# Performance work log

Measured on AMD Instinct MI355X. Metric: run time of the kernel, lower is better.

Reference implementation:

```python
import jax, jax.numpy as jnp
import numpy as np

B, IN_DIM, C, H, W = 4, 64, 128, 64, 64
HW = H * W
EPS = 1e-5


def _conv(x, w, b, pad):
    y = jax.lax.conv_general_dilated(
        x, w, (1, 1), [(pad, pad), (pad, pad)],
        dimension_numbers=('NCHW', 'OIHW', 'NCHW'))
    return y + b[None, :, None, None]


def _ln_chw(x, g, b):
    # torch LayerNorm([C,H,W]): normalize over (C,H,W) per sample, affine per-element
    m = jnp.mean(x, axis=(1, 2, 3), keepdims=True)
    v = jnp.mean((x - m) ** 2, axis=(1, 2, 3), keepdims=True)
    return (x - m) * jax.lax.rsqrt(v + EPS) * g[None] + b[None]


def _lrelu(x):
    return jnp.where(x >= 0, x, 0.01 * x)


def setup_inputs():
    ks = jax.random.split(jax.random.key(0), 16)

    def n(i, shape, s):
        return jax.random.normal(ks[i], shape, jnp.float32) * s

    inp = {
        'f_e': n(0, (B, IN_DIM, H, W), 1.0),
        'f_i': n(1, (B, IN_DIM, H, W), 1.0),
        'w1': n(2, (C, IN_DIM, 3, 3), 0.04), 'b1': jnp.zeros((C,), jnp.float32),
        'g1': jnp.ones((C, H, W), jnp.float32), 'be1': jnp.zeros((C, H, W), jnp.float32),
        'w2': n(3, (C, IN_DIM, 3, 3), 0.04), 'b2': jnp.zeros((C,), jnp.float32),
        'g2': jnp.ones((C, H, W), jnp.float32), 'be2': jnp.zeros((C, H, W), jnp.float32),
        'W3': n(4, (HW, HW), 0.015), 'b3': jnp.zeros((HW,), jnp.float32),
        'W4': n(5, (C, C), 0.08), 'b4': jnp.zeros((C,), jnp.float32),
        'W5': n(6, (C, C), 0.08), 'b5': jnp.zeros((C,), jnp.float32),
        'w6a': n(7, (C, C, 1, 1), 0.08), 'b6a': jnp.zeros((C,), jnp.float32),
        'g6a': jnp.ones((C, H, W), jnp.float32), 'be6a': jnp.zeros((C, H, W), jnp.float32),
        'w6b': n(8, (C, C, 3, 3), 0.03), 'b6b': jnp.zeros((C,), jnp.float32),
        'g6b': jnp.ones((C, H, W), jnp.float32), 'be6b': jnp.zeros((C, H, W), jnp.float32),
        'wf': n(9, (IN_DIM, C, 1, 1), 0.08), 'bf': jnp.zeros((IN_DIM,), jnp.float32),
    }
    return inp


def reference(f_e, f_i, w1, b1, g1, be1, w2, b2, g2, be2, W3, b3, W4, b4,
              W5, b5, w6a, b6a, g6a, be6a, w6b, b6b, g6b, be6b, wf, bf):
    b_, _, h, w = f_e.shape
    c = w1.shape[0]
    hw = h * w

    # f_1: conv3x3 -> LN([C,H,W]) -> LeakyReLU -> b (hw) c
    x1 = _lrelu(_ln_chw(_conv(f_e, w1, b1, 1), g1, be1))
    f_e_1 = x1.transpose(0, 2, 3, 1).reshape(b_, hw, c)

    # f_2: conv3x3 -> LN -> LeakyReLU (stays b c h w)
    f_i_2 = _lrelu(_ln_chw(_conv(f_i, w2, b2, 1), g2, be2))

    # f_3: b c (hw) -> Linear(HW,HW) -> LeakyReLU
    f_i_3 = _lrelu(jnp.einsum('bcn,mn->bcm', f_i_2.reshape(b_, c, hw), W3) + b3)

    # f_4: b (hw) c -> Linear(C,C) -> LeakyReLU
    tok = f_i_2.transpose(0, 2, 3, 1).reshape(b_, hw, c)
    f_e_4 = _lrelu(jnp.einsum('bnc,dc->bnd', tok, W4) + b4)

    # unscaled single-head attention over hw tokens
    scores = jnp.einsum('bnc,bcm->bnm', f_e_4, f_i_3)   # (b, hw, hw)
    attn = jax.nn.softmax(scores, axis=-1)
    f_e_5_in = jnp.einsum('bnm,bmc->bnc', attn, f_e_1)

    # f_5: Linear(C,C) -> LeakyReLU -> b c h w
    f_e_5 = _lrelu(jnp.einsum('bnc,dc->bnd', f_e_5_in, W5) + b5)
    f_e_5 = f_e_5.reshape(b_, h, w, c).transpose(0, 3, 1, 2)

    # f_6: conv1x1 -> LN -> LReLU -> conv3x3 -> LN -> LReLU
    y = _lrelu(_ln_chw(_conv(f_i_2, w6a, b6a, 0), g6a, be6a))
    f_i_6 = _lrelu(_ln_chw(_conv(y, w6b, b6b, 1), g6b, be6b))

    f_e_7 = f_e_5 * f_i_6
    f_e_8 = _conv(f_e_7, wf, bf, 0)
    return (f_e_8, f_i_2)
```

## Files before the change

kernel.cpp:

```cpp
#include <hip/hip_runtime.h>

typedef unsigned short ushort_t;
typedef unsigned int uint_t;
typedef unsigned long long u64_t;

#define Bn 4
#define IND 64
#define Cn 128
#define Nn 4096
#define CN 524288
#define BUF 2097152

typedef __attribute__((ext_vector_type(8))) __bf16 bf16x8;
typedef __attribute__((ext_vector_type(4))) float f32x4;

__device__ __forceinline__ float b2f(ushort_t s) {
    return __uint_as_float(((uint_t)s) << 16);
}
__device__ __forceinline__ ushort_t f2b(float f) {
    uint_t u = __float_as_uint(f);
    uint_t r = u + 0x7fffu + ((u >> 16) & 1u);
    return (ushort_t)(r >> 16);
}
__device__ __forceinline__ void unpack8(uint4 u, float* f) {
    f[0] = __uint_as_float(u.x << 16); f[1] = __uint_as_float(u.x & 0xffff0000u);
    f[2] = __uint_as_float(u.y << 16); f[3] = __uint_as_float(u.y & 0xffff0000u);
    f[4] = __uint_as_float(u.z << 16); f[5] = __uint_as_float(u.z & 0xffff0000u);
    f[6] = __uint_as_float(u.w << 16); f[7] = __uint_as_float(u.w & 0xffff0000u);
}
__device__ __forceinline__ float lrelu(float x) { return x >= 0.f ? x : 0.01f * x; }

__device__ __forceinline__ float getv(const float* p, size_t i) { return p[i]; }
__device__ __forceinline__ float getv(const ushort_t* p, size_t i) { return b2f(p[i]); }
__device__ __forceinline__ float4 get4(const float* p, size_t i) { return *(const float4*)(p + i); }
__device__ __forceinline__ float4 get4(const ushort_t* p, size_t i) {
    ushort4 u = *(const ushort4*)(p + i);
    float4 f = {b2f(u.x), b2f(u.y), b2f(u.z), b2f(u.w)};
    return f;
}
__device__ __forceinline__ void stv(float* p, float v) { *p = v; }
__device__ __forceinline__ void stv(ushort_t* p, float v) { *p = f2b(v); }

__device__ __forceinline__ uint4 pack8(float4 a, float4 b) {
    uint4 r;
    r.x = (uint_t)f2b(a.x) | ((uint_t)f2b(a.y) << 16);
    r.y = (uint_t)f2b(a.z) | ((uint_t)f2b(a.w) << 16);
    r.z = (uint_t)f2b(b.x) | ((uint_t)f2b(b.y) << 16);
    r.w = (uint_t)f2b(b.z) | ((uint_t)f2b(b.w) << 16);
    return r;
}

__global__ void detect_kernel(const void* g1, int* flag) {
    if (threadIdx.x == 0 && blockIdx.x == 0)
        *flag = (((const ushort_t*)g1)[0] == 0x3F80) ? 0 : 1;
}

template <int CI>
__global__ __launch_bounds__(256) void wtrans(const void* w, ushort_t* Wt, const int* flagp) {
    int F = *flagp;
    int idx = blockIdx.x * 256 + threadIdx.x;
    if (idx >= 128 * 9 * CI) return;
    int co = idx / (9 * CI);
    int rem = idx - co * 9 * CI;
    int tap = rem / CI;
    int ci = rem - tap * CI;
    size_t srci = (size_t)co * CI * 9 + (size_t)ci * 9 + tap;
    float v = F ? ((const float*)w)[srci] : b2f(((const ushort_t*)w)[srci]);
    Wt[idx] = f2b(v);
}

template <typename TEXT>
__device__ __forceinline__ void tin_body(const TEXT* src, ushort_t* dst, float (*tile)[33]) {
    int b = blockIdx.z, c0 = blockIdx.y * 32, n0 = blockIdx.x * 32;
    int nx = threadIdx.x & 31, cy = threadIdx.x >> 5;
    #pragma unroll
    for (int s = 0; s < 4; s++) {
        int cl = cy + s * 8;
        tile[cl][nx] = getv(src, ((size_t)(b * 64 + c0 + cl)) * 4096 + n0 + nx);
    }
    __syncthreads();
    #pragma unroll
    for (int s = 0; s < 4; s++) {
        int nl = cy + s * 8;
        dst[((size_t)b * 4096 + n0 + nl) * 64 + c0 + nx] = f2b(tile[nx][nl]);
    }
}

__global__ __launch_bounds__(256) void transpose_in(const void* src, ushort_t* dst, const int* flagp) {
    __shared__ float tile[32][33];
    int F = *flagp;
    if (F) tin_body((const float*)src, dst, tile);
    else   tin_body((const ushort_t*)src, dst, tile);
}

template <int CI>
__global__ __launch_bounds__(512) void conv_mfma(const ushort_t* __restrict__ Xt,
                                                 const ushort_t* __restrict__ Wt,
                                                 const void* bias, float* __restrict__ out,
                                                 const int* flagp) {
    constexpr int RS = CI + 8;
    constexpr int SROWS = 195;
    constexpr int SBYTES = SROWS * RS * 2;
    constexpr int OBYTES = 128 * 68 * 4;
    constexpr int SMEM = SBYTES > OBYTES ? SBYTES : OBYTES;
    __shared__ __align__(16) char smem[SMEM];
    ushort_t* S = (ushort_t*)smem;
    float* Ob = (float*)smem;

    int t = threadIdx.x;
    int blk = blockIdx.x;
    int b = blk >> 6, y = blk & 63;
    int n0 = y << 6;

    constexpr int RQ = CI / 8;
    constexpr int CNT = SROWS * RQ;
    for (int i = t; i < CNT; i += 512) {
        int s = i / RQ;
        int c8 = (i - s * RQ) * 8;
        int tok = n0 + s - 65;
        uint4 v = {0u, 0u, 0u, 0u};
        if (s < 194 && (unsigned)tok < 4096u)
            v = *(const uint4*)(Xt + ((size_t)b * 4096 + tok) * CI + c8);
        *(uint4*)(S + (size_t)s * RS + c8) = v;
    }
    __syncthreads();

    int lane = t & 63, w = t >> 6;
    int li = lane & 15, q = lane >> 4;
    int px0 = 16 * (w & 3);
    int coh = 64 * (w >> 2);
    int x = px0 + li;

    f32x4 acc[4];
    #pragma unroll
    for (int T = 0; T < 4; T++) acc[T] = {0.f, 0.f, 0.f, 0.f};

    #pragma unroll
    for (int tap = 0; tap < 9; tap++) {
        int dy = tap / 3 - 1, dx = tap % 3 - 1;
        bool vx = (unsigned)(x + dx) < 64u;
        int srow = x + dy * 64 + dx + 65;
        int sr2 = vx ? srow : 194;
        #pragma unroll
        for (int ks = 0; ks < CI / 32; ks++) {
            bf16x8 a = *(const bf16x8*)(S + (size_t)sr2 * RS + ks * 32 + q * 8);
            #pragma unroll
            for (int T = 0; T < 4; T++) {
                int co = coh + 16 * T + li;
                bf16x8 bb = *(const bf16x8*)(Wt + ((size_t)co * 9 + tap) * CI + ks * 32 + q * 8);
                acc[T] = __builtin_amdgcn_mfma_f32_16x16x32_bf16(a, bb, acc[T], 0, 0, 0);
            }
        }
    }
    __syncthreads();

    int F = *flagp;
    #pragma unroll
    for (int T = 0; T < 4; T++) {
        int co = coh + 16 * T + li;
        float bv = F ? ((const float*)bias)[co] : b2f(((const ushort_t*)bias)[co]);
        #pragma unroll
        for (int rr = 0; rr < 4; rr++)
            Ob[(size_t)co * 68 + px0 + 4 * q + rr] = acc[T][rr] + bv;
    }
    __syncthreads();
    for (int i = t; i < 2048; i += 512) {
        int co = i >> 4, p4 = (i & 15) * 4;
        *(uint4*)(out + ((size_t)(b * 128 + co)) * 4096 + n0 + p4) =
            *(const uint4*)(Ob + (size_t)co * 68 + p4);
    }
}

__global__ __launch_bounds__(256) void ln_reduce1(const float* __restrict__ src,
                                                  float* __restrict__ part) {
    int t = threadIdx.x;
    size_t base = (size_t)blockIdx.x * 1024 + t * 4;
    float4 v = *(const float4*)(src + base);
    float s = v.x + v.y + v.z + v.w;
    float q = v.x * v.x + v.y * v.y + v.z * v.z + v.w * v.w;
    for (int off = 32; off > 0; off >>= 1) {
        s += __shfl_down(s, off, 64);
        q += __shfl_down(q, off, 64);
    }
    __shared__ float red[8];
    if ((t & 63) == 0) { red[(t >> 6) * 2] = s; red[(t >> 6) * 2 + 1] = q; }
    __syncthreads();
    if (t == 0) {
        s = red[0] + red[2] + red[4] + red[6];
        q = red[1] + red[3] + red[5] + red[7];
        part[blockIdx.x * 2] = s;
        part[blockIdx.x * 2 + 1] = q;
    }
}

__global__ __launch_bounds__(256) void ln_reduce2(const float* __restrict__ part,
                                                  float* __restrict__ der) {
    int b = blockIdx.x, t = threadIdx.x;
    float s = part[(b * 512 + t) * 2] + part[(b * 512 + 256 + t) * 2];
    float q = part[(b * 512 + t) * 2 + 1] + part[(b * 512 + 256 + t) * 2 + 1];
    for (int off = 32; off > 0; off >>= 1) {
        s += __shfl_down(s, off, 64);
        q += __shfl_down(q, off, 64);
    }
    __shared__ float red[8];
    if ((t & 63) == 0) { red[(t >> 6) * 2] = s; red[(t >> 6) * 2 + 1] = q; }
    __syncthreads();
    if (t == 0) {
        s = red[0] + red[2] + red[4] + red[6];
        q = red[1] + red[3] + red[5] + red[7];
        float mean = s * (1.f / (float)CN);
        float var = q * (1.f / (float)CN) - mean * mean;
        der[b * 2] = mean;
        der[b * 2 + 1] = rsqrtf(var + 1e-5f);
    }
}

template <typename TEXT, typename TOD, int HT, int HD>
__device__ __forceinline__ void ln_body(const float* src, const TEXT* g, const TEXT* be,
                                        const float* der, ushort_t* outT, TOD* outD,
                                        float (*tile)[33]) {
    int b = blockIdx.z, c0 = blockIdx.y * 32, n0 = blockIdx.x * 32;
    float mean = der[b * 2], rstd = der[b * 2 + 1];
    int nx = threadIdx.x & 31, cy = threadIdx.x >> 5;
    #pragma unroll
    for (int s = 0; s < 4; s++) {
        int cl = cy + s * 8;
        int c = c0 + cl;
        size_t gi = (size_t)c * Nn + n0 + nx;
        float v = (src[(size_t)b * CN + gi] - mean) * rstd * getv(g, gi) + getv(be, gi);
        v = lrelu(v);
        if (HD) stv(outD + (size_t)b * CN + gi, v);
        tile[cl][nx] = v;
    }
    if (HT) {
        __syncthreads();
        #pragma unroll
        for (int s = 0; s < 4; s++) {
            int nl = cy + s * 8;
            int n = n0 + nl;
            int c = c0 + nx;
            outT[((size_t)b * Nn + n) * Cn + c] = f2b(tile[nx][nl]);
        }
    }
}

template <int HT, int HD, int DEXT>
__global__ __launch_bounds__(256) void ln_apply(const float* src, const void* g, const void* be,
                                                const float* der, ushort_t* outT, void* outD,
                                                long doff, const int* flagp) {
    __shared__ float tile[32][33];
    int F = *flagp;
    if (F) {
        if (DEXT && HD)
            ln_body<float, float, HT, HD>(src, (const float*)g, (const float*)be, der, outT,
                                          ((float*)outD) + doff, tile);
        else
            ln_body<float, ushort_t, HT, HD>(src, (const float*)g, (const float*)be, der, outT,
                                             ((ushort_t*)outD) + doff, tile);
    } else {
        ln_body<ushort_t, ushort_t, HT, HD>(src, (const ushort_t*)g, (const ushort_t*)be, der, outT,
                                            ((ushort_t*)outD) + doff, tile);
    }
}

template <int ACT, int TRANS, typename TA, typename TW, typename TO>
__device__ __forceinline__ void gemm_body(const TA* A, const TW* W, const TW* bias, TO* out,
                                          int M, int K, int Rper,
                                          float (*As)[68], float (*Bs)[68]) {
    int m0 = blockIdx.x << 6, r0 = blockIdx.y << 6;
    int t = threadIdx.x, tx = t & 15, ty = t >> 4;
    int sr = t >> 2, sk = (t & 3) << 2;
    float acc[4][4] = {{0.f}};
    for (int kt = 0; kt < K; kt += 16) {
        float4 av = get4(A, (size_t)(r0 + sr) * K + kt + sk);
        float4 wv = get4(W, (size_t)(m0 + sr) * K + kt + sk);
        As[sk + 0][sr] = av.x; As[sk + 1][sr] = av.y;
        As[sk + 2][sr] = av.z; As[sk + 3][sr] = av.w;
        Bs[sk + 0][sr] = wv.x; Bs[sk + 1][sr] = wv.y;
        Bs[sk + 2][sr] = wv.z; Bs[sk + 3][sr] = wv.w;
        __syncthreads();
        #pragma unroll
        for (int kk = 0; kk < 16; kk++) {
            float4 a4 = *(const float4*)&As[kk][ty << 2];
            float4 b4 = *(const float4*)&Bs[kk][tx << 2];
            float aa[4] = {a4.x, a4.y, a4.z, a4.w};
            float bb[4] = {b4.x, b4.y, b4.z, b4.w};
            #pragma unroll
            for (int ii = 0; ii < 4; ii++)
                #pragma unroll
                for (int jj = 0; jj < 4; jj++)
                    acc[ii][jj] += aa[ii] * bb[jj];
        }
        __syncthreads();
    }
    float bv[4];
    #pragma unroll
    for (int jj = 0; jj < 4; jj++) bv[jj] = getv(bias, m0 + (tx << 2) + jj);
    #pragma unroll
    for (int ii = 0; ii < 4; ii++) {
        int r = r0 + (ty << 2) + ii;
        float v[4];
        #pragma unroll
        for (int jj = 0; jj < 4; jj++) {
            float x = acc[ii][jj] + bv[jj];
            if (ACT) x = lrelu(x);
            v[jj] = x;
        }
        if (TRANS) {
            int rb = r / Rper, ri = r % Rper;
            #pragma unroll
            for (int jj = 0; jj < 4; jj++) {
                int m = m0 + (tx << 2) + jj;
                stv(out + ((size_t)rb * M + m) * Rper + ri, v[jj]);
            }
        } else {
            #pragma unroll
            for (int jj = 0; jj < 4; jj++)
                stv(out + (size_t)r * M + m0 + (tx << 2) + jj, v[jj]);
        }
    }
}

template <int ACT, int TRANS, int AK, typename TO>
__global__ __launch_bounds__(256) void gemm_nt(const void* A, long aoff, const void* W,
                                               const void* bias, TO* out, int M, int K, int Rper,
                                               const int* flagp) {
    __shared__ float As[16][68];
    __shared__ float Bs[16][68];
    int F = *flagp;
    if (AK == 0) {
        if (F) gemm_body<ACT, TRANS>((const ushort_t*)A + aoff, (const float*)W, (const float*)bias, out, M, K, Rper, As, Bs);
        else   gemm_body<ACT, TRANS>((const ushort_t*)A + aoff, (const ushort_t*)W, (const ushort_t*)bias, out, M, K, Rper, As, Bs);
    } else if (AK == 1) {
        if (F) gemm_body<ACT, TRANS>((const float*)A + aoff, (const float*)W, (const float*)bias, out, M, K, Rper, As, Bs);
        else   gemm_body<ACT, TRANS>((const float*)A + aoff, (const ushort_t*)W, (const ushort_t*)bias, out, M, K, Rper, As, Bs);
    } else {
        if (F) gemm_body<ACT, TRANS>((const float*)A + aoff, (const float*)W, (const float*)bias, out, M, K, Rper, As, Bs);
        else   gemm_body<ACT, TRANS>((const ushort_t*)A + aoff, (const ushort_t*)W, (const ushort_t*)bias, out, M, K, Rper, As, Bs);
    }
}

template <typename TA, typename TW>
__device__ __forceinline__ void gemm_big_body(const TA* A, const TW* W3, const TW* b3,
                                              ushort_t* out, char* smem) {
    ushort_t* As = (ushort_t*)smem;
    ushort_t* Bs = (ushort_t*)(smem + 9216);
    int t = threadIdx.x;
    int m0 = blockIdx.x << 7;
    int r0 = blockIdx.y << 6;
    int lane = t & 63, w = t >> 6;
    int li = lane & 15, q = lane >> 4;
    int rs = 16 * (w & 3);
    int mh = 64 * (w >> 2);
    f32x4 acc[4];
    #pragma unroll
    for (int T = 0; T < 4; T++) acc[T] = {0.f, 0.f, 0.f, 0.f};

    int ar = t >> 3, ak8 = (t & 7) * 8;
    int br = t >> 2, bk16 = (t & 3) * 16;

    {
        size_t abase = (size_t)(r0 + ar) * 4096 + ak8;
        *(uint4*)(As + (size_t)ar * 72 + ak8) = pack8(get4(A, abase), get4(A, abase + 4));
        size_t bbase = (size_t)(m0 + br) * 4096 + bk16;
        *(uint4*)(Bs + (size_t)br * 72 + bk16) = pack8(get4(W3, bbase), get4(W3, bbase + 4));
        *(uint4*)(Bs + (size_t)br * 72 + bk16 + 8) = pack8(get4(W3, bbase + 8), get4(W3, bbase + 12));
    }
    __syncthreads();

    for (int kt = 0; kt < 4096; kt += 64) {
        float4 pa0, pa1, pb0, pb1, pb2, pb3;
        bool pf = kt < 4032;
        if (pf) {
            size_t abase = (size_t)(r0 + ar) * 4096 + kt + 64 + ak8;
            pa0 = get4(A, abase); pa1 = get4(A, abase + 4);
            size_t bbase = (size_t)(m0 + br) * 4096 + kt + 64 + bk16;
            pb0 = get4(W3, bbase); pb1 = get4(W3, bbase + 4);
            pb2 = get4(W3, bbase + 8); pb3 = get4(W3, bbase + 12);
        }
        #pragma unroll
        for (int ks = 0; ks < 2; ks++) {
            bf16x8 a = *(const bf16x8*)(As + (size_t)(rs + li) * 72 + ks * 32 + q * 8);
            #pragma unroll
            for (int T = 0; T < 4; T++) {
                bf16x8 bb = *(const bf16x8*)(Bs + (size_t)(mh + 16 * T + li) * 72 + ks * 32 + q * 8);
                acc[T] = __builtin_amdgcn_mfma_f32_16x16x32_bf16(a, bb, acc[T], 0, 0, 0);
            }
        }
        __syncthreads();
        if (pf) {
            *(uint4*)(As + (size_t)ar * 72 + ak8) = pack8(pa0, pa1);
            *(uint4*)(Bs + (size_t)br * 72 + bk16) = pack8(pb0, pb1);
            *(uint4*)(Bs + (size_t)br * 72 + bk16 + 8) = pack8(pb2, pb3);
        }
        __syncthreads();
    }

    ushort_t* Ob = (ushort_t*)smem;
    #pragma unroll
    for (int T = 0; T < 4; T++) {
        int m_l = mh + 16 * T + li;
        float bv = getv(b3, m0 + m_l);
        #pragma unroll
        for (int rr = 0; rr < 4; rr++) {
            float v = lrelu(acc[T][rr] + bv);
            Ob[(size_t)m_l * 72 + rs + 4 * q + rr] = f2b(v);
        }
    }
    __syncthreads();
    int b = r0 >> 7;
    int c0 = ((r0 >> 6) & 1) * 64;
    for (int i = t; i < 1024; i += 512) {
        int m_l = i >> 3, c8 = (i & 7) * 8;
        *(uint4*)(out + ((size_t)b * 4096 + m0 + m_l) * 128 + c0 + c8) =
            *(const uint4*)(Ob + (size_t)m_l * 72 + c8);
    }
}

__global__ __launch_bounds__(512) void gemm_big(const void* A, long aoff, const void* W3,
                                                const void* b3, ushort_t* out, const int* flagp) {
    __shared__ __align__(16) char smem[27648];
    int F = *flagp;
    if (F) gemm_big_body((const float*)A + aoff, (const float*)W3, (const float*)b3, out, smem);
    else   gemm_big_body((const ushort_t*)A + aoff, (const ushort_t*)W3, (const ushort_t*)b3, out, smem);
}

__global__ __launch_bounds__(256, 2) void attn_mfma(const ushort_t* __restrict__ Q,
                                                    const ushort_t* __restrict__ Kg,
                                                    const ushort_t* __restrict__ Vg,
                                                    ushort_t* __restrict__ Op0,
                                                    ushort_t* __restrict__ Op1,
                                                    ushort_t* __restrict__ Op2,
                                                    ushort_t* __restrict__ Op3,
                                                    float* __restrict__ ML) {
    __shared__ __align__(16) ushort_t Ks[64 * 136];
    __shared__ __align__(16) ushort_t Vt[128 * 72];
    __shared__ __align__(16) ushort_t Ps[128 * 88];

    int t = threadIdx.x;
    int blk = blockIdx.x;
    int h = blk >> 7;
    int rblk = blk & 127;
    int b = rblk & 3;
    int qt = rblk >> 2;
    int n0 = qt << 7;
    int lane = t & 63, w = t >> 6;
    int li = lane & 15, q = lane >> 4;

    int kj = t >> 2, kc0 = (t & 3) * 32;
    int vd = t >> 1, vk0 = (t & 1) * 32;

    int kt0 = h << 4;
    int m00 = kt0 << 6;

    {
        const ushort_t* kp = Kg + ((size_t)(b * Nn + m00 + kj)) * 128 + kc0;
        ushort_t* dst = Ks + kj * 136 + kc0;
        #pragma unroll
        for (int cc = 0; cc < 4; cc++)
            *(uint4*)(dst + cc * 8) = *(const uint4*)(kp + cc * 8);
    }
    {
        const ushort_t* vp = Vg + (size_t)b * CN + (size_t)vd * Nn + m00 + vk0;
        ushort_t* dst = Vt + vd * 72 + vk0;
        #pragma unroll
        for (int cc = 0; cc < 4; cc++)
            *(uint4*)(dst + cc * 8) = *(const uint4*)(vp + cc * 8);
    }

    bf16x8 qf[2][4];
    #pragma unroll
    for (int sub = 0; sub < 2; sub++)
        #pragma unroll
        for (int ks = 0; ks < 4; ks++)
            qf[sub][ks] = *(const bf16x8*)(Q +
                ((size_t)(b * Nn + n0 + 32 * w + 16 * sub + li)) * 128 + ks * 32 + q * 8);

    f32x4 acc[2][8];
    #pragma unroll
    for (int sub = 0; sub < 2; sub++)
        #pragma unroll
        for (int T = 0; T < 8; T++) acc[sub][T] = {0.f, 0.f, 0.f, 0.f};
    float m_i[2][4], l_i[2][4];
    #pragma unroll
    for (int sub = 0; sub < 2; sub++)
        #pragma unroll
        for (int r = 0; r < 4; r++) { m_i[sub][r] = -1e30f; l_i[sub][r] = 0.f; }

    __syncthreads();

    for (int kt = kt0; kt < kt0 + 16; kt++) {
        uint4 pk[4], pv[4];
        bool pf = kt < kt0 + 15;
        if (pf) {
            int m1 = (kt + 1) << 6;
            const ushort_t* kp = Kg + ((size_t)(b * Nn + m1 + kj)) * 128 + kc0;
            #pragma unroll
            for (int cc = 0; cc < 4; cc++) pk[cc] = *(const uint4*)(kp + cc * 8);
            const ushort_t* vp = Vg + (size_t)b * CN + (size_t)vd * Nn + m1 + vk0;
            #pragma unroll
            for (int cc = 0; cc < 4; cc++) pv[cc] = *(const uint4*)(vp + cc * 8);
        }

        f32x4 s[2][4];
        #pragma unroll
        for (int sub = 0; sub < 2; sub++)
            #pragma unroll
            for (int T = 0; T < 4; T++) s[sub][T] = {0.f, 0.f, 0.f, 0.f};
        __builtin_amdgcn_s_setprio(1);
        #pragma unroll
        for (int ks = 0; ks < 4; ks++) {
            bf16x8 a0 = qf[0][ks];
            bf16x8 a1 = qf[1][ks];
            #pragma unroll
            for (int T = 0; T < 4; T++) {
                bf16x8 kb = *(const bf16x8*)(Ks + (16 * T + li) * 136 + ks * 32 + q * 8);
                s[0][T] = __builtin_amdgcn_mfma_f32_16x16x32_bf16(a0, kb, s[0][T], 0, 0, 0);
                s[1][T] = __builtin_amdgcn_mfma_f32_16x16x32_bf16(a1, kb, s[1][T], 0, 0, 0);
            }
        }
        __builtin_amdgcn_s_setprio(0);

        float rm[2][4];
        bool grow = false;
        #pragma unroll
        for (int sub = 0; sub < 2; sub++)
            #pragma unroll
            for (int r = 0; r < 4; r++) {
                float v = fmaxf(fmaxf(s[sub][0][r], s[sub][1][r]),
                                fmaxf(s[sub][2][r], s[sub][3][r]));
                v = fmaxf(v, __shfl_xor(v, 1, 64));
                v = fmaxf(v, __shfl_xor(v, 2, 64));
                v = fmaxf(v, __shfl_xor(v, 4, 64));
                v = fmaxf(v, __shfl_xor(v, 8, 64));
                rm[sub][r] = v;
                grow = grow || (v > m_i[sub][r]);
            }
        if (__any(grow)) {
            #pragma unroll
            for (int sub = 0; sub < 2; sub++)
                #pragma unroll
                for (int r = 0; r < 4; r++) {
                    float mnew = fmaxf(m_i[sub][r], rm[sub][r]);
                    float al = __expf(m_i[sub][r] - mnew);
                    m_i[sub][r] = mnew;
                    float rsum = 0.f;
                    #pragma unroll
                    for (int T = 0; T < 4; T++) {
                        float pvv = __expf(s[sub][T][r] - mnew);
                        Ps[(32 * w + 16 * sub + 4 * q + r) * 88 + 16 * T + li] = f2b(pvv);
                        rsum += pvv;
                    }
                    l_i[sub][r] = l_i[sub][r] * al + rsum;
                    #pragma unroll
                    for (int T = 0; T < 8; T++) acc[sub][T][r] *= al;
                }
        } else {
            #pragma unroll
            for (int sub = 0; sub < 2; sub++)
                #pragma unroll
                for (int r = 0; r < 4; r++) {
                    float rsum = 0.f;
                    #pragma unroll
                    for (int T = 0; T < 4; T++) {
                        float pvv = __expf(s[sub][T][r] - m_i[sub][r]);
                        Ps[(32 * w + 16 * sub + 4 * q + r) * 88 + 16 * T + li] = f2b(pvv);
                        rsum += pvv;
                    }
                    l_i[sub][r] += rsum;
                }
        }

        __builtin_amdgcn_s_setprio(1);
        #pragma unroll
        for (int ks = 0; ks < 2; ks++) {
            bf16x8 pa0 = *(const bf16x8*)(Ps + (32 * w + li) * 88 + ks * 32 + q * 8);
            bf16x8 pa1 = *(const bf16x8*)(Ps + (32 * w + 16 + li) * 88 + ks * 32 + q * 8);
            #pragma unroll
            for (int T = 0; T < 8; T++) {
                bf16x8 vb = *(const bf16x8*)(Vt + (16 * T + li) * 72 + ks * 32 + q * 8);
                acc[0][T] = __builtin_amdgcn_mfma_f32_16x16x32_bf16(pa0, vb, acc[0][T], 0, 0, 0);
                acc[1][T] = __builtin_amdgcn_mfma_f32_16x16x32_bf16(pa1, vb, acc[1][T], 0, 0, 0);
            }
        }
        __builtin_amdgcn_s_setprio(0);
        __syncthreads();
        if (pf) {
            ushort_t* dk = Ks + kj * 136 + kc0;
            #pragma unroll
            for (int cc = 0; cc < 4; cc++) *(uint4*)(dk + cc * 8) = pk[cc];
            ushort_t* dv = Vt + vd * 72 + vk0;
            #pragma unroll
            for (int cc = 0; cc < 4; cc++) *(uint4*)(dv + cc * 8) = pv[cc];
            __syncthreads();
        }
    }

    #pragma unroll
    for (int sub = 0; sub < 2; sub++)
        #pragma unroll
        for (int r = 0; r < 4; r++) {
            float ls = l_i[sub][r];
            ls += __shfl_xor(ls, 1, 64);
            ls += __shfl_xor(ls, 2, 64);
            ls += __shfl_xor(ls, 4, 64);
            ls += __shfl_xor(ls, 8, 64);
            l_i[sub][r] = ls;
        }

    ushort_t* Op = (h == 0) ? Op0 : (h == 1) ? Op1 : (h == 2) ? Op2 : Op3;
    #pragma unroll
    for (int sub = 0; sub < 2; sub++)
        #pragma unroll
        for (int T = 0; T < 8; T++)
            #pragma unroll
            for (int r = 0; r < 4; r++) {
                int n = n0 + 32 * w + 16 * sub + 4 * q + r;
                int d = 16 * T + li;
                Op[((size_t)(b * Nn + n)) * 128 + d] = f2b(acc[sub][T][r]);
            }
    if (li == 0) {
        #pragma unroll
        for (int sub = 0; sub < 2; sub++)
            #pragma unroll
            for (int r = 0; r < 4; r++) {
                int n = n0 + 32 * w + 16 * sub + 4 * q + r;
                size_t mi = ((size_t)(h * Bn + b) * Nn + n) * 2;
                ML[mi] = m_i[sub][r];
                ML[mi + 1] = l_i[sub][r];
            }
    }
}

__global__ __launch_bounds__(256) void attn_merge(const ushort_t* __restrict__ Op0,
                                                  const ushort_t* __restrict__ Op1,
                                                  const ushort_t* __restrict__ Op2,
                                                  const ushort_t* __restrict__ Op3,
                                                  const float* __restrict__ ML,
                                                  float* __restrict__ Og) {
    int idx = blockIdx.x * 256 + threadIdx.x;
    int token = idx >> 4;
    int c8 = (idx & 15) * 8;
    float m[4], l[4];
    #pragma unroll
    for (int s = 0; s < 4; s++) {
        m[s] = ML[((size_t)s * (Bn * Nn) + token) * 2];
        l[s] = ML[((size_t)s * (Bn * Nn) + token) * 2 + 1];
    }
    float M = fmaxf(fmaxf(m[0], m[1]), fmaxf(m[2], m[3]));
    float e[4];
    float denom = 0.f;
    #pragma unroll
    for (int s = 0; s < 4; s++) { e[s] = __expf(m[s] - M); denom += l[s] * e[s]; }
    float inv = 1.f / denom;
    #pragma unroll
    for (int s = 0; s < 4; s++) e[s] *= inv;
    uint4 u0 = *(const uint4*)(Op0 + (size_t)token * 128 + c8);
    uint4 u1 = *(const uint4*)(Op1 + (size_t)token * 128 + c8);
    uint4 u2 = *(const uint4*)(Op2 + (size_t)token * 128 + c8);
    uint4 u3 = *(const uint4*)(Op3 + (size_t)token * 128 + c8);
    float f0[8], f1[8], f2[8], f3[8];
    unpack8(u0, f0);
    unpack8(u1, f1);
    unpack8(u2, f2);
    unpack8(u3, f3);
    float o[8];
    #pragma unroll
    for (int j = 0; j < 8; j++)
        o[j] = f0[j] * e[0] + f1[j] * e[1] + f2[j] * e[2] + f3[j] * e[3];
    float4 v0 = {o[0], o[1], o[2], o[3]};
    float4 v1 = {o[4], o[5], o[6], o[7]};
    float* op = Og + (size_t)token * 128 + c8;
    *(float4*)op = v0;
    *(float4*)(op + 4) = v1;
}

template <typename TEXT, typename TOUT>
__device__ __forceinline__ void final_body(const ushort_t* fe5, const ushort_t* fi6t,
                                           const TEXT* wf, const TEXT* bf, TOUT* out0,
                                           float* prod, ushort_t* wfs, float* bfs) {
    int t = threadIdx.x;
    int b = blockIdx.x >> 6;
    int px0 = (blockIdx.x & 63) * 64;
    for (int idx = t * 4; idx < 8192; idx += 1024) {
        float4 v = get4(wf, idx);
        ushort4 u = {f2b(v.x), f2b(v.y), f2b(v.z), f2b(v.w)};
        *(ushort4*)&wfs[idx] = u;
    }
    if (t < 64) bfs[t] = getv(bf, t);
    {
        int pix = t >> 2, kc = (t & 3) * 32;
        const ushort_t* ap = fe5 + ((size_t)(b * Nn + px0 + pix)) * 128 + kc;
        const ushort_t* bp = fi6t + ((size_t)(b * Nn + px0 + pix)) * 128 + kc;
        #pragma unroll
        for (int c = 0; c < 4; c++) {
            uint4 ua = *(const uint4*)(ap + c * 8);
            uint4 ub = *(const uint4*)(bp + c * 8);
            float fa[8], fb[8];
            unpack8(ua, fa);
            unpack8(ub, fb);
            float* pp = &prod[pix * 132 + kc + c * 8];
            #pragma unroll
            for (int j = 0; j < 8; j++) pp[j] = fa[j] * fb[j];
        }
    }
    __syncthreads();
    int pix = t >> 2, og = t & 3;
    for (int k = 0; k < 16; k++) {
        int o = og * 16 + k;
        float a = bfs[o];
        for (int kc = 0; kc < 128; kc += 8) {
            uint4 wu = *(const uint4*)&wfs[o * 128 + kc];
            float w8[8];
            unpack8(wu, w8);
            const float* pp = &prod[pix * 132 + kc];
            float4 p0 = *(const float4*)pp;
            float4 p1 = *(const float4*)(pp + 4);
            a += w8[0] * p0.x + w8[1] * p0.y + w8[2] * p0.z + w8[3] * p0.w
               + w8[4] * p1.x + w8[5] * p1.y + w8[6] * p1.z + w8[7] * p1.w;
        }
        stv(out0 + ((size_t)(b * 64 + o)) * Nn + px0 + pix, a);
    }
}

__global__ __launch_bounds__(256) void final_out(const ushort_t* fe5, const ushort_t* fi6t,
                                                 const void* wf, const void* bf, void* out0,
                                                 const int* flagp) {
    __shared__ __align__(16) float prod[64 * 132];
    __shared__ __align__(16) ushort_t wfs[64 * 128];
    __shared__ float bfs[64];
    int F = *flagp;
    if (F) final_body((const ushort_t*)fe5, fi6t, (const float*)wf, (const float*)bf, (float*)out0, prod, wfs, bfs);
    else   final_body((const ushort_t*)fe5, fi6t, (const ushort_t*)wf, (const ushort_t*)bf, (ushort_t*)out0, prod, wfs, bfs);
}

extern "C" void kernel_launch(void* const* d_in, const int* in_sizes, int n_in,
                              void* d_out, int out_size, void* d_ws, size_t ws_size,
                              hipStream_t stream) {
    const void* f_e = d_in[0];
    const void* f_i = d_in[1];
    const void* w1 = d_in[2];
    const void* b1 = d_in[3];
    const void* g1 = d_in[4];
    const void* be1 = d_in[5];
    const void* w2 = d_in[6];
    const void* b2 = d_in[7];
    const void* g2 = d_in[8];
    const void* be2 = d_in[9];
    const void* W3 = d_in[10];
    const void* b3 = d_in[11];
    const void* W4 = d_in[12];
    const void* b4 = d_in[13];
    const void* W5 = d_in[14];
    const void* b5 = d_in[15];
    const void* w6a = d_in[16];
    const void* b6a = d_in[17];
    const void* g6a = d_in[18];
    const void* be6a = d_in[19];
    const void* w6b = d_in[20];
    const void* b6b = d_in[21];
    const void* g6b = d_in[22];
    const void* be6b = d_in[23];
    const void* wf = d_in[24];
    const void* bf = d_in[25];

    char* wsb = (char*)d_ws;
    int* FLAG = (int*)wsb;
    float* PART = (float*)(wsb + 1024);
    float* DER  = (float*)(wsb + 17408);
    ushort_t* Wt1  = (ushort_t*)(wsb + 32768);
    ushort_t* Wt2  = (ushort_t*)(wsb + 180224);
    ushort_t* Wt6b = (ushort_t*)(wsb + 327680);
    float* ML   = (float*)(wsb + 32768);
    float* TMP  = (float*)(wsb + 622592);
    ushort_t* FE1  = (ushort_t*)(wsb + 9011200);
    ushort_t* TOK  = FE1 + BUF;
    ushort_t* FI3T = TOK + BUF;
    ushort_t* FE4  = FI3T + BUF;
    ushort_t* Y6   = FE4 + BUF;
    ushort_t* FI6T = Y6 + BUF;

    ushort_t* FEt = FI3T;
    ushort_t* FIt = FE4;

    ushort_t* OPA = (ushort_t*)TMP;
    ushort_t* OPB = OPA + BUF;
    float* MRG = (float*)FI3T;

    const long OUT1OFF = (long)Bn * IND * Nn;

    dim3 lnGrid(128, 4, 4);
    dim3 tinGrid(128, 2, 4);

    detect_kernel<<<1, 64, 0, stream>>>(g1, FLAG);

    wtrans<64><<<288, 256, 0, stream>>>(w1, Wt1, FLAG);
    wtrans<64><<<288, 256, 0, stream>>>(w2, Wt2, FLAG);
    wtrans<128><<<576, 256, 0, stream>>>(w6b, Wt6b, FLAG);

    transpose_in<<<tinGrid, 256, 0, stream>>>(f_e, FEt, FLAG);
    conv_mfma<64><<<256, 512, 0, stream>>>(FEt, Wt1, b1, TMP, FLAG);
    ln_reduce1<<<2048, 256, 0, stream>>>(TMP, PART);
    ln_reduce2<<<4, 256, 0, stream>>>(PART, DER);
    ln_apply<0, 1, 0><<<lnGrid, 256, 0, stream>>>(TMP, g1, be1, DER, nullptr, FE1, 0, FLAG);

    transpose_in<<<tinGrid, 256, 0, stream>>>(f_i, FIt, FLAG);
    conv_mfma<64><<<256, 512, 0, stream>>>(FIt, Wt2, b2, TMP, FLAG);
    ln_reduce1<<<2048, 256, 0, stream>>>(TMP, PART);
    ln_reduce2<<<4, 256, 0, stream>>>(PART, DER);
    ln_apply<1, 1, 1><<<lnGrid, 256, 0, stream>>>(TMP, g2, be2, DER, TOK, d_out, OUT1OFF, FLAG);

    gemm_big<<<dim3(32, 8), 512, 0, stream>>>(d_out, OUT1OFF, W3, b3, FI3T, FLAG);

    gemm_nt<1, 0, 0, ushort_t><<<dim3(2, 256), 256, 0, stream>>>(TOK, 0, W4, b4, FE4, 128, 128, 1, FLAG);

    gemm_nt<0, 1, 0, float><<<dim3(2, 256), 256, 0, stream>>>(TOK, 0, w6a, b6a, TMP, 128, 128, 4096, FLAG);
    ln_reduce1<<<2048, 256, 0, stream>>>(TMP, PART);
    ln_reduce2<<<4, 256, 0, stream>>>(PART, DER);
    ln_apply<1, 0, 0><<<lnGrid, 256, 0, stream>>>(TMP, g6a, be6a, DER, Y6, nullptr, 0, FLAG);

    conv_mfma<128><<<256, 512, 0, stream>>>(Y6, Wt6b, b6b, TMP, FLAG);
    ln_reduce1<<<2048, 256, 0, stream>>>(TMP, PART);
    ln_reduce2<<<4, 256, 0, stream>>>(PART, DER);
    ln_apply<1, 0, 0><<<lnGrid, 256, 0, stream>>>(TMP, g6b, be6b, DER, FI6T, nullptr, 0, FLAG);

    attn_mfma<<<512, 256, 0, stream>>>(FE4, FI3T, FE1, TOK, Y6, OPA, OPB, ML);
    attn_merge<<<1024, 256, 0, stream>>>(TOK, Y6, OPA, OPB, ML, MRG);

    gemm_nt<1, 0, 1, ushort_t><<<dim3(2, 256), 256, 0, stream>>>(MRG, 0, W5, b5, Y6, 128, 128, 1, FLAG);

    final_out<<<256, 256, 0, stream>>>(Y6, FI6T, wf, bf, d_out, FLAG);
}
```

Before: 569.5 us.

## Restructure W3 GEMM with larger tiles, split-K, and separate bf16 conversion

```diff
diff --git a/kernel.cpp b/kernel.cpp
--- a/kernel.cpp
+++ b/kernel.cpp
@@ -340,89 +340,145 @@
     }
 }
 
-template <typename TA, typename TW>
-__device__ __forceinline__ void gemm_big_body(const TA* A, const TW* W3, const TW* b3,
-                                              ushort_t* out, char* smem) {
-    ushort_t* As = (ushort_t*)smem;
-    ushort_t* Bs = (ushort_t*)(smem + 9216);
+__global__ __launch_bounds__(256) void a_convert(const void* src, long aoff, ushort_t* dst,
+                                                 const int* flagp) {
+    int F = *flagp;
+    size_t idx = (size_t)blockIdx.x * 256 + threadIdx.x;
+    if (F) {
+        const float* s = (const float*)src + aoff;
+        float4 a = *(const float4*)(s + idx * 8);
+        float4 b = *(const float4*)(s + idx * 8 + 4);
+        *(uint4*)(dst + idx * 8) = pack8(a, b);
+    } else {
+        const uint4* s = (const uint4*)((const ushort_t*)src + aoff);
+        *(uint4*)(dst + idx * 8) = s[idx];
+    }
+}
+
+__global__ __launch_bounds__(512) void gemm_big2(const ushort_t* __restrict__ Ap,
+                                                 const void* __restrict__ W3,
+                                                 float* __restrict__ C00, float* __restrict__ C01,
+                                                 float* __restrict__ C10, float* __restrict__ C11,
+                                                 const int* flagp) {
+    __shared__ __align__(16) char smem[73728];
+    ushort_t* Als = (ushort_t*)smem;
+    ushort_t* Bls = (ushort_t*)(smem + 36864);
+    float* Ot = (float*)smem;
+
+    int F = *flagp;
     int t = threadIdx.x;
-    int m0 = blockIdx.x << 7;
-    int r0 = blockIdx.y << 6;
+    int m0 = blockIdx.x << 6;
+    int rb = blockIdx.y;
+    int ksl = blockIdx.z;
+    size_t kbase = (size_t)ksl * 2048;
+
     int lane = t & 63, w = t >> 6;
     int li = lane & 15, q = lane >> 4;
-    int rs = 16 * (w & 3);
-    int mh = 64 * (w >> 2);
-    f32x4 acc[4];
-    #pragma unroll
-    for (int T = 0; T < 4; T++) acc[T] = {0.f, 0.f, 0.f, 0.f};
-
-    int ar = t >> 3, ak8 = (t & 7) * 8;
-    int br = t >> 2, bk16 = (t & 3) * 16;
+    int wr = w & 3, wc = w >> 2;
+
+    int ar = t >> 1, ak = (t & 1) * 32;
+    int br = t >> 3, bk = (t & 7) * 8;
+
+    const ushort_t* Abase = Ap + ((size_t)(rb * 256 + ar)) * 4096 + kbase + ak;
+    const float* Wf = (const float*)W3 + ((size_t)(m0 + br)) * 4096 + kbase + bk;
+    const ushort_t* Wh = (const ushort_t*)W3 + ((size_t)(m0 + br)) * 4096 + kbase + bk;
+
+    f32x4 acc[4][2];
+    #pragma unroll
+    for (int i = 0; i < 4; i++)
+        #pragma unroll
+        for (int j = 0; j < 2; j++) acc[i][j] = {0.f, 0.f, 0.f, 0.f};
 
     {
-        size_t abase = (size_t)(r0 + ar) * 4096 + ak8;
-        *(uint4*)(As + (size_t)ar * 72 + ak8) = pack8(get4(A, abase), get4(A, abase + 4));
-        size_t bbase = (size_t)(m0 + br) * 4096 + bk16;
-        *(uint4*)(Bs + (size_t)br * 72 + bk16) = pack8(get4(W3, bbase), get4(W3, bbase + 4));
-        *(uint4*)(Bs + (size_t)br * 72 + bk16 + 8) = pack8(get4(W3, bbase + 8), get4(W3, bbase + 12));
-    }
-    __syncthreads();
-
-    for (int kt = 0; kt < 4096; kt += 64) {
-        float4 pa0, pa1, pb0, pb1, pb2, pb3;
-        bool pf = kt < 4032;
+        #pragma unroll
+        for (int cc = 0; cc < 4; cc++)
+            *(uint4*)(Als + (size_t)ar * 72 + ak + cc * 8) = *(const uint4*)(Abase + cc * 8);
+        if (F) *(uint4*)(Bls + (size_t)br * 72 + bk) = pack8(*(const float4*)Wf, *(const float4*)(Wf + 4));
+        else   *(uint4*)(Bls + (size_t)br * 72 + bk) = *(const uint4*)Wh;
+    }
+    __syncthreads();
+
+    for (int kt = 0; kt < 2048; kt += 64) {
+        uint4 pa[4];
+        float4 pb0, pb1;
+        uint4 pbu;
+        bool pf = kt < 1984;
         if (pf) {
-            size_t abase = (size_t)(r0 + ar) * 4096 + kt + 64 + ak8;
-            pa0 = get4(A, abase); pa1 = get4(A, abase + 4);
-            size_t bbase = (size_t)(m0 + br) * 4096 + kt + 64 + bk16;
-            pb0 = get4(W3, bbase); pb1 = get4(W3, bbase + 4);
-            pb2 = get4(W3, bbase + 8); pb3 = get4(W3, bbase + 12);
-        }
+            #pragma unroll
+            for (int cc = 0; cc < 4; cc++)
+                pa[cc] = *(const uint4*)(Abase + kt + 64 + cc * 8);
+            if (F) { pb0 = *(const float4*)(Wf + kt + 64); pb1 = *(const float4*)(Wf + kt + 68); }
+            else   { pbu = *(const uint4*)(Wh + kt + 64); }
+        }
+        __builtin_amdgcn_s_setprio(1);
         #pragma unroll
         for (int ks = 0; ks < 2; ks++) {
-            bf16x8 a = *(const bf16x8*)(As + (size_t)(rs + li) * 72 + ks * 32 + q * 8);
-            #pragma unroll
-            for (int T = 0; T < 4; T++) {
-                bf16x8 bb = *(const bf16x8*)(Bs + (size_t)(mh + 16 * T + li) * 72 + ks * 32 + q * 8);
-                acc[T] = __builtin_amdgcn_mfma_f32_16x16x32_bf16(a, bb, acc[T], 0, 0, 0);
-            }
-        }
+            bf16x8 af[4], bfr[2];
+            #pragma unroll
+            for (int rf = 0; rf < 4; rf++)
+                af[rf] = *(const bf16x8*)(Als + (size_t)(64 * wr + 16 * rf + li) * 72 + ks * 32 + q * 8);
+            #pragma unroll
+            for (int cf = 0; cf < 2; cf++)
+                bfr[cf] = *(const bf16x8*)(Bls + (size_t)(32 * wc + 16 * cf + li) * 72 + ks * 32 + q * 8);
+            #pragma unroll
+            for (int rf = 0; rf < 4; rf++)
+                #pragma unroll
+                for (int cf = 0; cf < 2; cf++)
+                    acc[rf][cf] = __builtin_amdgcn_mfma_f32_16x16x32_bf16(af[rf], bfr[cf], acc[rf][cf], 0, 0, 0);
+        }
+        __builtin_amdgcn_s_setprio(0);
         __syncthreads();
         if (pf) {
-            *(uint4*)(As + (size_t)ar * 72 + ak8) = pack8(pa0, pa1);
-            *(uint4*)(Bs + (size_t)br * 72 + bk16) = pack8(pb0, pb1);
-            *(uint4*)(Bs + (size_t)br * 72 + bk16 + 8) = pack8(pb2, pb3);
-        }
-        __syncthreads();
-    }
-
-    ushort_t* Ob = (ushort_t*)smem;
-    #pragma unroll
-    for (int T = 0; T < 4; T++) {
-        int m_l = mh + 16 * T + li;
-        float bv = getv(b3, m0 + m_l);
-        #pragma unroll
-        for (int rr = 0; rr < 4; rr++) {
-            float v = lrelu(acc[T][rr] + bv);
-            Ob[(size_t)m_l * 72 + rs + 4 * q + rr] = f2b(v);
-        }
-    }
-    __syncthreads();
-    int b = r0 >> 7;
-    int c0 = ((r0 >> 6) & 1) * 64;
-    for (int i = t; i < 1024; i += 512) {
-        int m_l = i >> 3, c8 = (i & 7) * 8;
-        *(uint4*)(out + ((size_t)b * 4096 + m0 + m_l) * 128 + c0 + c8) =
-            *(const uint4*)(Ob + (size_t)m_l * 72 + c8);
-    }
-}
-
-__global__ __launch_bounds__(512) void gemm_big(const void* A, long aoff, const void* W3,
-                                                const void* b3, ushort_t* out, const int* flagp) {
-    __shared__ __align__(16) char smem[27648];
+            #pragma unroll
+            for (int cc = 0; cc < 4; cc++)
+                *(uint4*)(Als + (size_t)ar * 72 + ak + cc * 8) = pa[cc];
+            if (F) *(uint4*)(Bls + (size_t)br * 72 + bk) = pack8(pb0, pb1);
+            else   *(uint4*)(Bls + (size_t)br * 72 + bk) = pbu;
+            __syncthreads();
+        }
+    }
+
+    #pragma unroll
+    for (int rf = 0; rf < 4; rf++)
+        #pragma unroll
+        for (int cf = 0; cf < 2; cf++)
+            #pragma unroll
+            for (int rr = 0; rr < 4; rr++)
+                Ot[(size_t)(64 * wr + 16 * rf + 4 * q + rr) * 72 + 32 * wc + 16 * cf + li] = acc[rf][cf][rr];
+    __syncthreads();
+    float* Pc = (rb == 0) ? (ksl == 0 ? C00 : C01) : (ksl == 0 ? C10 : C11);
+    for (int g = t; g < 4096; g += 512) {
+        int row = g >> 4, c4 = (g & 15) * 4;
+        *(float4*)(Pc + (size_t)row * 4096 + m0 + c4) = *(const float4*)(Ot + (size_t)row * 72 + c4);
+    }
+}
+
+__global__ __launch_bounds__(256) void gemm_merge(const float* __restrict__ C00,
+                                                  const float* __restrict__ C01,
+                                                  const float* __restrict__ C10,
+                                                  const float* __restrict__ C11,
+                                                  const void* b3, ushort_t* __restrict__ out,
+                                                  const int* flagp) {
+    __shared__ float tile[32][33];
     int F = *flagp;
-    if (F) gemm_big_body((const float*)A + aoff, (const float*)W3, (const float*)b3, out, smem);
-    else   gemm_big_body((const ushort_t*)A + aoff, (const ushort_t*)W3, (const ushort_t*)b3, out, smem);
+    int m0 = blockIdx.x * 32, c0 = blockIdx.y * 32, b = blockIdx.z;
+    const float* P0 = (b < 2) ? C00 : C10;
+    const float* P1 = (b < 2) ? C01 : C11;
+    int rbase = (b & 1) * 128;
+    int nx = threadIdx.x & 31, cy = threadIdx.x >> 5;
+    float bv = F ? ((const float*)b3)[m0 + nx] : b2f(((const ushort_t*)b3)[m0 + nx]);
+    #pragma unroll
+    for (int s = 0; s < 4; s++) {
+        int cl = cy + s * 8;
+        size_t ri = (size_t)(rbase + c0 + cl) * 4096 + m0 + nx;
+        tile[cl][nx] = lrelu(P0[ri] + P1[ri] + bv);
+    }
+    __syncthreads();
+    #pragma unroll
+    for (int s = 0; s < 4; s++) {
+        int ml = cy + s * 8;
+        out[((size_t)b * 4096 + m0 + ml) * 128 + c0 + nx] = f2b(tile[nx][ml]);
+    }
 }
 
 __global__ __launch_bounds__(256, 2) void attn_mfma(const ushort_t* __restrict__ Q,
@@ -783,6 +839,12 @@
     ushort_t* FEt = FI3T;
     ushort_t* FIt = FE4;
 
+    float* C00 = TMP;
+    float* C01 = TMP + (BUF / 2);
+    float* C10 = (float*)FE4;
+    float* C11 = (float*)Y6;
+    ushort_t* ABF = FI6T;
+
     ushort_t* OPA = (ushort_t*)TMP;
     ushort_t* OPB = OPA + BUF;
     float* MRG = (float*)FI3T;
@@ -810,7 +872,9 @@
     ln_reduce2<<<4, 256, 0, stream>>>(PART, DER);
     ln_apply<1, 1, 1><<<lnGrid, 256, 0, stream>>>(TMP, g2, be2, DER, TOK, d_out, OUT1OFF, FLAG);
 
-    gemm_big<<<dim3(32, 8), 512, 0, stream>>>(d_out, OUT1OFF, W3, b3, FI3T, FLAG);
+    a_convert<<<1024, 256, 0, stream>>>(d_out, OUT1OFF, ABF, FLAG);
+    gemm_big2<<<dim3(64, 2, 2), 512, 0, stream>>>(ABF, W3, C00, C01, C10, C11, FLAG);
+    gemm_merge<<<dim3(128, 4, 4), 256, 0, stream>>>(C00, C01, C10, C11, b3, FI3T, FLAG);
 
     gemm_nt<1, 0, 0, ushort_t><<<dim3(2, 256), 256, 0, stream>>>(TOK, 0, W4, b4, FE4, 128, 128, 1, FLAG);
 
```

Result: no change. 560.7 us (-1.5%).
